# Optimization experiments

Hardware: AMD Instinct MI355X
Metric: run time of the kernel (lower is better)

Reference implementation:

```python
import jax, jax.numpy as jnp
import numpy as np

N, E, C, H, G = 100000, 1600000, 128, 64, 512
TOL = 1e-7          # PyG topk tolerance
MIN_SCORE = 0.05
EPS_KL = 1e-14


def setup_inputs() -> dict:
    key = jax.random.key(0)
    ks = jax.random.split(key, 12)
    d = {}
    d["x"] = jax.random.normal(ks[0], (N, C), jnp.float32)
    d["edge_index"] = jax.random.randint(ks[1], (2, E), 0, N)
    d["batch"] = jnp.sort(jax.random.randint(ks[2], (N,), 0, G))
    d["attn"] = jax.random.uniform(ks[3], (N,), jnp.float32, minval=1e-3, maxval=1.0)
    def lin(k, i, o):
        return (jax.random.normal(k, (i, o), jnp.float32) / np.sqrt(i)).astype(jnp.float32)
    d["W1"] = lin(ks[4], C, H); d["b1"] = jnp.zeros((H,), jnp.float32)
    d["W2"] = lin(ks[5], H, H); d["b2"] = jnp.zeros((H,), jnp.float32)
    d["pool_w"] = (jax.random.normal(ks[6], (C,), jnp.float32) / np.sqrt(C)).astype(jnp.float32)
    d["W3"] = lin(ks[7], H, H); d["b3"] = jnp.zeros((H,), jnp.float32)
    d["W4"] = lin(ks[8], H, H); d["b4"] = jnp.zeros((H,), jnp.float32)
    d["Wl"] = lin(ks[9], H, 1); d["bl"] = jnp.zeros((1,), jnp.float32)
    return d


def _gin(x, src, dst, Wa, ba, Wb, bb, edge_w=None):
    # GINConv with eps=0: nn((1+0)*x + sum_{j in N(i)} x_j), nn = Lin-ReLU-Lin
    msg = x[src]                                   # [E, F] gather
    if edge_w is not None:
        msg = msg * edge_w[:, None]                # drop pruned edges
    agg = jax.ops.segment_sum(msg, dst, num_segments=x.shape[0])
    h = x + agg
    return jax.nn.relu(h @ Wa + ba) @ Wb + bb


def reference(x, edge_index, batch, attn, W1, b1, W2, b2, pool_w, W3, b3, W4, b4, Wl, bl):
    src, dst = edge_index[0], edge_index[1]
    out = jax.nn.relu(_gin(x, src, dst, W1, b1, W2, b2))

    # --- TopKPooling(min_score=0.05), attn=x ---
    raw = x @ pool_w                               # [N] attention logits
    m = jax.ops.segment_max(raw, batch, num_segments=G)
    e = jnp.exp(raw - m[batch])
    z = jax.ops.segment_sum(e, batch, num_segments=G)
    score = e / z[batch]                           # per-graph softmax
    smax = jax.ops.segment_max(score, batch, num_segments=G)
    thresh = jnp.minimum(smax[batch] - TOL, MIN_SCORE)
    mask = score > thresh                          # kept nodes (>=1 per graph)
    maskf = mask.astype(x.dtype)
    out = out * (score * maskf)[:, None]           # x[perm] * score[perm]
    edge_keep = maskf[src] * maskf[dst]            # filter_adj: both endpoints kept

    out = jax.nn.relu(_gin(out, src, dst, W3, b3, W4, b4, edge_w=edge_keep)) * maskf[:, None]
    graph_out = jax.ops.segment_sum(out, batch, num_segments=G)  # global_add_pool
    pred = (graph_out @ Wl + bl).reshape(-1)       # [G]

    # attn_loss = scatter_mean(kl_div(log(score+eps), attn[perm]), batch)
    kl = attn * (jnp.log(attn) - jnp.log(score + EPS_KL))
    cnt = jax.ops.segment_sum(maskf, batch, num_segments=G)
    attn_loss = jax.ops.segment_sum(kl * maskf, batch, num_segments=G) / jnp.maximum(cnt, 1.0)

    ratio = maskf.sum() / x.shape[0]
    return pred, attn_loss, ratio
```

## Files before the change

kernel.cpp:

```cpp
#include <hip/hip_runtime.h>
#include <math.h>

#define N_NODES 100000
#define N_EDGES 1600000
#define C_IN    128
#define H_DIM   64
#define G_GRAPHS 512
#define MAXG    4096
#define ELCAP   65536
#define KPG     32
#define NBITS   3136

__global__ void kpre(const float* __restrict__ x, const float* __restrict__ pool_w,
                     const int* __restrict__ batch,
                     float* __restrict__ sc, unsigned int* __restrict__ zero_region,
                     int* __restrict__ gstart) {
    int gid = blockIdx.x * blockDim.x + threadIdx.x;
    int nthr = gridDim.x * blockDim.x;
    if (gid < NBITS + 1) zero_region[gid] = 0u;
    for (int i = gid; i < N_NODES; i += nthr) {
        int b = batch[i];
        int prev = (i == 0) ? -1 : batch[i - 1];
        for (int g = prev + 1; g <= b; ++g) gstart[g] = i;
    }
    if (gid == 0) {
        int last = batch[N_NODES - 1];
        for (int g = last + 1; g <= G_GRAPHS; ++g) gstart[g] = N_NODES;
    }
    const int lane = threadIdx.x & 63;
    const int l32  = lane & 31;
    const int half = lane >> 5;
    const float4 pwv = ((const float4*)pool_w)[l32];
    const int wid = blockIdx.x * (blockDim.x >> 6) + (threadIdx.x >> 6);
    const int nw  = gridDim.x * (blockDim.x >> 6);
    for (int r0 = wid * 4; r0 < N_NODES; r0 += nw * 4) {
        int rowA = r0 + half;
        int rowB = r0 + 2 + half;
        float4 xa = ((const float4*)(x + (size_t)rowA * C_IN))[l32];
        float4 xb = ((const float4*)(x + (size_t)rowB * C_IN))[l32];
        float pa = xa.x * pwv.x + xa.y * pwv.y + xa.z * pwv.z + xa.w * pwv.w;
        float pb = xb.x * pwv.x + xb.y * pwv.y + xb.z * pwv.z + xb.w * pwv.w;
        #pragma unroll
        for (int m = 16; m > 0; m >>= 1) {
            pa += __shfl_xor(pa, m, 64);
            pb += __shfl_xor(pb, m, 64);
        }
        if (l32 == 0) { sc[rowA] = pa; sc[rowB] = pb; }
    }
}

__device__ __forceinline__ float blk_max(float v, float* red, int lane, int w) {
    #pragma unroll
    for (int m = 32; m > 0; m >>= 1) v = fmaxf(v, __shfl_xor(v, m, 64));
    if (lane == 0) red[w] = v;
    __syncthreads();
    float r = fmaxf(fmaxf(red[0], red[1]), fmaxf(red[2], red[3]));
    __syncthreads();
    return r;
}
__device__ __forceinline__ float blk_sum(float v, float* red, int lane, int w) {
    #pragma unroll
    for (int m = 32; m > 0; m >>= 1) v += __shfl_xor(v, m, 64);
    if (lane == 0) red[w] = v;
    __syncthreads();
    float r = (red[0] + red[1]) + (red[2] + red[3]);
    __syncthreads();
    return r;
}

__global__ void kA4(const int* __restrict__ gstart, const float* __restrict__ attn,
                    float* __restrict__ sc, unsigned int* __restrict__ kept_bits,
                    int* __restrict__ klist, int* __restrict__ kcnt,
                    float* __restrict__ B, float* __restrict__ out) {
    __shared__ float buf[MAXG];
    __shared__ float red[4];
    __shared__ int   lst[KPG];
    __shared__ int   cntk;
    const int g = blockIdx.x;
    const int t = threadIdx.x;
    const int lane = t & 63;
    const int w = t >> 6;
    const int ns = gstart[g];
    const int ne = gstart[g + 1];
    const int cn = ne - ns;
    if (cn <= 0) {
        if (t == 0) { out[G_GRAPHS + g] = 0.f; kcnt[g] = 0; }
        return;
    }
    if (t == 0) cntk = 0;
    float lmax = -3.4e38f;
    for (int i = t; i < cn; i += 256) { float r = sc[ns + i]; buf[i] = r; lmax = fmaxf(lmax, r); }
    float m = blk_max(lmax, red, lane, w);
    float lsum = 0.f;
    for (int i = t; i < cn; i += 256) { float e = expf(buf[i] - m); buf[i] = e; lsum += e; }
    float z = blk_sum(lsum, red, lane, w);
    float thresh = fminf(1.f / z - 1e-7f, 0.05f);
    float klacc = 0.f;
    for (int i = t; i < cn; i += 256) {
        float s = buf[i] / z;
        if (s > thresh) {
            int n = ns + i;
            int p = atomicAdd(&cntk, 1);
            if (p < KPG) lst[p] = i;
            sc[n] = s;
            float a = attn[n];
            klacc += a * (logf(a) - logf(s + 1e-14f));
        }
    }
    float klsum = blk_sum(klacc, red, lane, w);
    int kct = cntk;
    int kc = kct < KPG ? kct : KPG;
    if (t == 0) {
        out[G_GRAPHS + g] = (kct > 0) ? klsum / (float)kct : 0.f;
        kcnt[g] = kc;
    }
    for (int i = t; i < kc; i += 256) {
        int n = ns + lst[i];
        klist[g * KPG + i] = n;
        atomicOr(&kept_bits[n >> 5], 1u << (n & 31));
    }
    for (int j = t; j < kc * H_DIM; j += 256)
        B[(size_t)(ns + lst[j >> 6]) * H_DIM + (j & 63)] = 0.f;
}

__device__ __forceinline__ void emit(bool hit, int s, int d, int* __restrict__ list,
                                     int cap, int* __restrict__ count, int lane) {
    unsigned long long bal = __ballot(hit);
    if (bal == 0ull) return;
    int leader = __ffsll((long long)bal) - 1;
    int cnt = __popcll(bal);
    int base = 0;
    if (lane == leader) base = atomicAdd(count, cnt);
    base = __shfl(base, leader, 64);
    if (hit) {
        int p = base + __popcll(bal & ((1ull << lane) - 1ull));
        if (p < cap) { list[p] = s; list[cap + p] = d; }
    }
}

__global__ void kscan(const int* __restrict__ ei, const unsigned int* __restrict__ bits,
                      const float* __restrict__ x, const float* __restrict__ W1,
                      float* __restrict__ B, int* __restrict__ elsd,
                      int* __restrict__ elcount) {
    __shared__ int ls[1024], ld[1024];
    __shared__ int c1;
    const int t = threadIdx.x;
    const int lane = t & 63;
    if (t == 0) c1 = 0;
    int t4 = blockIdx.x * 256 + t;
    bool valid = t4 < (N_EDGES / 4);
    int4 s4 = make_int4(0, 0, 0, 0), d4 = make_int4(0, 0, 0, 0);
    if (valid) {
        s4 = ((const int4*)ei)[t4];
        d4 = ((const int4*)(ei + N_EDGES))[t4];
    }
    __syncthreads();
    int sv[4] = {s4.x, s4.y, s4.z, s4.w};
    int dv[4] = {d4.x, d4.y, d4.z, d4.w};
    bool bk[4];
    #pragma unroll
    for (int q = 0; q < 4; ++q) {
        int ss = sv[q], dd = dv[q];
        bool kd = valid && (((bits[dd >> 5] >> (dd & 31)) & 1u) != 0u);
        bk[q] = kd && (((bits[ss >> 5] >> (ss & 31)) & 1u) != 0u);
        if (kd) { int p = atomicAdd(&c1, 1); ls[p] = ss; ld[p] = dd; }
    }
    #pragma unroll
    for (int q = 0; q < 4; ++q) emit(bk[q], sv[q], dv[q], elsd, ELCAP, elcount, lane);
    __syncthreads();
    const int nloc = c1;
    if (nloc == 0) return;
    const int w = t >> 6;
    for (int idx = w; idx < nloc; idx += 4) {
        int s = ls[idx];
        int d = ld[idx];
        const float4* xr = (const float4*)(x + (size_t)s * C_IN);
        float acc = 0.f;
        #pragma unroll 8
        for (int k4 = 0; k4 < C_IN / 4; ++k4) {
            float4 xv = xr[k4];
            acc = fmaf(xv.x, W1[(4 * k4 + 0) * H_DIM + lane], acc);
            acc = fmaf(xv.y, W1[(4 * k4 + 1) * H_DIM + lane], acc);
            acc = fmaf(xv.z, W1[(4 * k4 + 2) * H_DIM + lane], acc);
            acc = fmaf(xv.w, W1[(4 * k4 + 3) * H_DIM + lane], acc);
        }
        atomicAdd(&B[(size_t)d * H_DIM + lane], acc);
    }
}

__device__ __forceinline__ float computeA(int n, int lane,
                                          const float* __restrict__ x,
                                          const float* __restrict__ B,
                                          const float* __restrict__ sc,
                                          const float* __restrict__ W1, float b1l,
                                          const float* __restrict__ W2, float b2l,
                                          const float* __restrict__ W3) {
    const float4* xr = (const float4*)(x + (size_t)n * C_IN);
    float u = 0.f;
    #pragma unroll 8
    for (int k4 = 0; k4 < C_IN / 4; ++k4) {
        float4 xv = xr[k4];
        u = fmaf(xv.x, W1[(4 * k4 + 0) * H_DIM + lane], u);
        u = fmaf(xv.y, W1[(4 * k4 + 1) * H_DIM + lane], u);
        u = fmaf(xv.z, W1[(4 * k4 + 2) * H_DIM + lane], u);
        u = fmaf(xv.w, W1[(4 * k4 + 3) * H_DIM + lane], u);
    }
    float t1 = fmaxf(u + B[(size_t)n * H_DIM + lane] + b1l, 0.f);
    float o1 = b2l;
    #pragma unroll 8
    for (int k = 0; k < H_DIM; ++k) o1 = fmaf(__shfl(t1, k, 64), W2[k * H_DIM + lane], o1);
    o1 = fmaxf(o1, 0.f);
    float v = 0.f;
    #pragma unroll 8
    for (int k = 0; k < H_DIM; ++k) v = fmaf(__shfl(o1, k, 64), W3[k * H_DIM + lane], v);
    return v * sc[n];
}

__global__ void kfin(const int* __restrict__ klist, const int* __restrict__ kcnt,
                     const float* __restrict__ sc, const float* __restrict__ x,
                     const float* __restrict__ W1, const float* __restrict__ b1,
                     const float* __restrict__ W2, const float* __restrict__ b2,
                     const float* __restrict__ W3, const float* __restrict__ b3,
                     const float* __restrict__ W4, const float* __restrict__ b4,
                     const float* __restrict__ Wl, const float* __restrict__ bl,
                     const float* __restrict__ B, const int* __restrict__ elsd,
                     const int* __restrict__ elcount, float* __restrict__ out) {
    __shared__ float Abuf[KPG][H_DIM];
    __shared__ float Gbuf[KPG][H_DIM];
    __shared__ int   kl_s[KPG];
    const int g = blockIdx.x;
    const int t = threadIdx.x;
    const int lane = t & 63;
    const int w = t >> 6;
    const float b1l = b1[lane], b2l = b2[lane];
    const int kc = kcnt[g];
    if (t < KPG) kl_s[t] = (t < kc) ? klist[g * KPG + t] : 0;
    __syncthreads();
    int ec = *elcount; if (ec > ELCAP) ec = ELCAP;
    for (int i = w; i < kc; i += 4) {
        int n = __builtin_amdgcn_readfirstlane(kl_s[i]);
        float vA = computeA(n, lane, x, B, sc, W1, b1l, W2, b2l, W3);
        float agg = 0.f;
        for (int base = 0; base < ec; base += 64) {
            int idx = base + lane;
            int dd = (idx < ec) ? elsd[ELCAP + idx] : -1;
            bool mtc = (dd == n);
            int ssl = mtc ? elsd[idx] : 0;
            unsigned long long bal = __ballot(mtc);
            while (bal) {
                int j = __ffsll((long long)bal) - 1;
                bal &= bal - 1;
                int s = __builtin_amdgcn_readfirstlane(__shfl(ssl, j, 64));
                agg += computeA(s, lane, x, B, sc, W1, b1l, W2, b2l, W3);
            }
        }
        Abuf[i][lane] = vA;
        Gbuf[i][lane] = agg;
    }
    __syncthreads();
    if (w == 0) {
        const float b3l = b3[lane], b4l = b4[lane];
        float gsum = 0.f;
        for (int i = 0; i < kc; ++i) {
            float tt = fmaxf(Abuf[i][lane] + Gbuf[i][lane] + b3l, 0.f);
            float o2 = b4l;
            #pragma unroll 8
            for (int k = 0; k < H_DIM; ++k)
                o2 = fmaf(__shfl(tt, k, 64), W4[k * H_DIM + lane], o2);
            gsum += fmaxf(o2, 0.f);
        }
        float p = gsum * Wl[lane];
        #pragma unroll
        for (int m = 32; m > 0; m >>= 1) p += __shfl_xor(p, m, 64);
        if (lane == 0) out[g] = p + bl[0];
    }
    if (g == 0 && w == 1) {
        int tot = 0;
        for (int i = lane; i < G_GRAPHS; i += 64) tot += kcnt[i];
        #pragma unroll
        for (int m = 32; m > 0; m >>= 1) tot += __shfl_xor(tot, m, 64);
        if (lane == 0) out[2 * G_GRAPHS] = (float)tot * (1.f / (float)N_NODES);
    }
}

extern "C" void kernel_launch(void* const* d_in, const int* in_sizes, int n_in,
                              void* d_out, int out_size, void* d_ws, size_t ws_size,
                              hipStream_t stream) {
    const float* x      = (const float*)d_in[0];
    const int*   ei     = (const int*)d_in[1];
    const int*   batch  = (const int*)d_in[2];
    const float* attn   = (const float*)d_in[3];
    const float* W1     = (const float*)d_in[4];
    const float* b1     = (const float*)d_in[5];
    const float* W2     = (const float*)d_in[6];
    const float* b2     = (const float*)d_in[7];
    const float* pool_w = (const float*)d_in[8];
    const float* W3     = (const float*)d_in[9];
    const float* b3     = (const float*)d_in[10];
    const float* W4     = (const float*)d_in[11];
    const float* b4     = (const float*)d_in[12];
    const float* Wl     = (const float*)d_in[13];
    const float* bl     = (const float*)d_in[14];
    float* out = (float*)d_out;

    float* B      = (float*)d_ws;
    float* sc     = B + (size_t)N_NODES * H_DIM;
    int*   klist  = (int*)(sc + N_NODES);
    int*   kcnt   = klist + G_GRAPHS * KPG;
    int*   elsd   = kcnt + G_GRAPHS;
    unsigned int* kept_bits = (unsigned int*)(elsd + 2 * ELCAP);
    int*          elcount   = (int*)(kept_bits + NBITS);
    int*          gstart    = elcount + 1;

    kpre  <<<2048, 256, 0, stream>>>(x, pool_w, batch, sc, kept_bits, gstart);
    kA4   <<<G_GRAPHS, 256, 0, stream>>>(gstart, attn, sc, kept_bits, klist, kcnt, B, out);
    kscan <<<(N_EDGES / 4 + 255) / 256, 256, 0, stream>>>(ei, kept_bits, x, W1, B,
                                                          elsd, elcount);
    kfin  <<<G_GRAPHS, 256, 0, stream>>>(klist, kcnt, sc, x, W1, b1, W2, b2, W3, b3,
                                         W4, b4, Wl, bl, B, elsd, elcount, out);
}
```

Baseline: 168.1 us.

## Fuse score projection and per-graph softmax into one per-graph kernel

Merges the pre-pass kernel (x·pool_w projection, graph-start computation, bitmask zeroing) into the per-graph softmax/top-k kernel. Each 1024-thread block now finds its graph range with a wave-level binary search over the sorted batch array, clears its own bits of the kept bitmask with atomicAnd, and computes the logits straight into shared memory. This removes one launch and the round trip of the logits through global memory. In exchange only 512 blocks read x, with fewer waves in flight than the 2048-block pre-pass, and clearing bits per graph may leave some words uncleared if any graph is empty.

```diff
diff --git a/kernel.cpp b/kernel.cpp
--- a/kernel.cpp
+++ b/kernel.cpp
@@ -11,67 +11,40 @@
 #define KPG     32
 #define NBITS   3136
 
-__global__ void kpre(const float* __restrict__ x, const float* __restrict__ pool_w,
-                     const int* __restrict__ batch,
-                     float* __restrict__ sc, unsigned int* __restrict__ zero_region,
-                     int* __restrict__ gstart) {
-    int gid = blockIdx.x * blockDim.x + threadIdx.x;
-    int nthr = gridDim.x * blockDim.x;
-    if (gid < NBITS + 1) zero_region[gid] = 0u;
-    for (int i = gid; i < N_NODES; i += nthr) {
-        int b = batch[i];
-        int prev = (i == 0) ? -1 : batch[i - 1];
-        for (int g = prev + 1; g <= b; ++g) gstart[g] = i;
-    }
-    if (gid == 0) {
-        int last = batch[N_NODES - 1];
-        for (int g = last + 1; g <= G_GRAPHS; ++g) gstart[g] = N_NODES;
-    }
-    const int lane = threadIdx.x & 63;
-    const int l32  = lane & 31;
-    const int half = lane >> 5;
-    const float4 pwv = ((const float4*)pool_w)[l32];
-    const int wid = blockIdx.x * (blockDim.x >> 6) + (threadIdx.x >> 6);
-    const int nw  = gridDim.x * (blockDim.x >> 6);
-    for (int r0 = wid * 4; r0 < N_NODES; r0 += nw * 4) {
-        int rowA = r0 + half;
-        int rowB = r0 + 2 + half;
-        float4 xa = ((const float4*)(x + (size_t)rowA * C_IN))[l32];
-        float4 xb = ((const float4*)(x + (size_t)rowB * C_IN))[l32];
-        float pa = xa.x * pwv.x + xa.y * pwv.y + xa.z * pwv.z + xa.w * pwv.w;
-        float pb = xb.x * pwv.x + xb.y * pwv.y + xb.z * pwv.z + xb.w * pwv.w;
-        #pragma unroll
-        for (int m = 16; m > 0; m >>= 1) {
-            pa += __shfl_xor(pa, m, 64);
-            pb += __shfl_xor(pb, m, 64);
-        }
-        if (l32 == 0) { sc[rowA] = pa; sc[rowB] = pb; }
-    }
-}
-
-__device__ __forceinline__ float blk_max(float v, float* red, int lane, int w) {
-    #pragma unroll
-    for (int m = 32; m > 0; m >>= 1) v = fmaxf(v, __shfl_xor(v, m, 64));
-    if (lane == 0) red[w] = v;
-    __syncthreads();
-    float r = fmaxf(fmaxf(red[0], red[1]), fmaxf(red[2], red[3]));
-    __syncthreads();
-    return r;
-}
-__device__ __forceinline__ float blk_sum(float v, float* red, int lane, int w) {
-    #pragma unroll
-    for (int m = 32; m > 0; m >>= 1) v += __shfl_xor(v, m, 64);
-    if (lane == 0) red[w] = v;
-    __syncthreads();
-    float r = (red[0] + red[1]) + (red[2] + red[3]);
-    __syncthreads();
-    return r;
-}
-
-__global__ void kA4(const int* __restrict__ gstart, const float* __restrict__ attn,
-                    float* __restrict__ sc, unsigned int* __restrict__ kept_bits,
-                    int* __restrict__ klist, int* __restrict__ kcnt,
-                    float* __restrict__ B, float* __restrict__ out) {
+__device__ __forceinline__ int lbound64(const int* __restrict__ b, int val, int lane) {
+    int lo = 0, hi = N_NODES;
+    while (lo < hi) {
+        int len = hi - lo;
+        if (len <= 64) {
+            int p = lo + lane;
+            bool c = (p >= hi) || (b[p] >= val);
+            unsigned long long bal = __ballot(c);
+            lo = (bal == 0ull) ? hi : lo + (__ffsll((long long)bal) - 1);
+            hi = lo;
+        } else {
+            int step = len >> 6;
+            int p = lo + lane * step;
+            bool c = b[p] >= val;
+            unsigned long long bal = __ballot(c);
+            if (bal == 0ull) {
+                lo = lo + 63 * step + 1;
+            } else {
+                int j = __ffsll((long long)bal) - 1;
+                if (j == 0) { hi = lo; }
+                else { int nlo = lo + (j - 1) * step + 1; hi = lo + j * step; lo = nlo; }
+            }
+        }
+    }
+    return lo;
+}
+
+__global__ __launch_bounds__(1024, 4) void kSM(
+    const float* __restrict__ x, const int* __restrict__ batch,
+    const float* __restrict__ attn, const float* __restrict__ pool_w,
+    float* __restrict__ sc, unsigned int* __restrict__ kept_bits,
+    int* __restrict__ klist, int* __restrict__ kcnt,
+    float* __restrict__ B, int* __restrict__ elcount, float* __restrict__ out)
+{
     __shared__ float buf[MAXG];
     __shared__ float red[4];
     __shared__ int   lst[KPG];
@@ -79,47 +52,96 @@
     const int g = blockIdx.x;
     const int t = threadIdx.x;
     const int lane = t & 63;
-    const int w = t >> 6;
-    const int ns = gstart[g];
-    const int ne = gstart[g + 1];
+    const int w64 = t >> 6;
+    if (g == 0 && t == 0) *elcount = 0;
+    if (t == 0) cntk = 0;
+
+    const int ns = lbound64(batch, g, lane);
+    const int ne = lbound64(batch, g + 1, lane);
     const int cn = ne - ns;
     if (cn <= 0) {
         if (t == 0) { out[G_GRAPHS + g] = 0.f; kcnt[g] = 0; }
         return;
     }
-    if (t == 0) cntk = 0;
+
+    {
+        const int w0 = ns >> 5, w1 = (ne - 1) >> 5;
+        for (int wd = w0 + t; wd <= w1; wd += 1024) {
+            int lo_b = ns - (wd << 5); if (lo_b < 0) lo_b = 0;
+            int hi_b = ne - (wd << 5); if (hi_b > 32) hi_b = 32;
+            unsigned int mask = (hi_b == 32 ? 0xFFFFFFFFu : ((1u << hi_b) - 1u))
+                                & ~((1u << lo_b) - 1u);
+            atomicAnd(&kept_bits[wd], ~mask);
+        }
+    }
+
+    {
+        const int l32  = lane & 31;
+        const int half = lane >> 5;
+        const int hw   = (w64 << 1) + half;
+        const float4 pwv = ((const float4*)pool_w)[l32];
+        for (int r = ns + hw; r < ne; r += 32) {
+            float4 xa = ((const float4*)(x + (size_t)r * C_IN))[l32];
+            float pa = xa.x * pwv.x + xa.y * pwv.y + xa.z * pwv.z + xa.w * pwv.w;
+            #pragma unroll
+            for (int m = 16; m > 0; m >>= 1) pa += __shfl_xor(pa, m, 64);
+            if (l32 == 0) buf[r - ns] = pa;
+        }
+    }
+    __syncthreads();
+
     float lmax = -3.4e38f;
-    for (int i = t; i < cn; i += 256) { float r = sc[ns + i]; buf[i] = r; lmax = fmaxf(lmax, r); }
-    float m = blk_max(lmax, red, lane, w);
+    if (t < 256) for (int i = t; i < cn; i += 256) lmax = fmaxf(lmax, buf[i]);
+    #pragma unroll
+    for (int m = 32; m > 0; m >>= 1) lmax = fmaxf(lmax, __shfl_xor(lmax, m, 64));
+    if (t < 256 && lane == 0) red[w64] = lmax;
+    __syncthreads();
+    const float mx = fmaxf(fmaxf(red[0], red[1]), fmaxf(red[2], red[3]));
+    __syncthreads();
+
     float lsum = 0.f;
-    for (int i = t; i < cn; i += 256) { float e = expf(buf[i] - m); buf[i] = e; lsum += e; }
-    float z = blk_sum(lsum, red, lane, w);
-    float thresh = fminf(1.f / z - 1e-7f, 0.05f);
+    if (t < 256) for (int i = t; i < cn; i += 256) {
+        float e = expf(buf[i] - mx); buf[i] = e; lsum += e;
+    }
+    #pragma unroll
+    for (int m = 32; m > 0; m >>= 1) lsum += __shfl_xor(lsum, m, 64);
+    if (t < 256 && lane == 0) red[w64] = lsum;
+    __syncthreads();
+    const float z = (red[0] + red[1]) + (red[2] + red[3]);
+    __syncthreads();
+
+    const float thresh = fminf(1.f / z - 1e-7f, 0.05f);
     float klacc = 0.f;
-    for (int i = t; i < cn; i += 256) {
-        float s = buf[i] / z;
-        if (s > thresh) {
-            int n = ns + i;
-            int p = atomicAdd(&cntk, 1);
-            if (p < KPG) lst[p] = i;
-            sc[n] = s;
-            float a = attn[n];
-            klacc += a * (logf(a) - logf(s + 1e-14f));
-        }
-    }
-    float klsum = blk_sum(klacc, red, lane, w);
+    if (t < 256) {
+        for (int i = t; i < cn; i += 256) {
+            float s = buf[i] / z;
+            if (s > thresh) {
+                int n = ns + i;
+                int p = atomicAdd(&cntk, 1);
+                if (p < KPG) lst[p] = i;
+                sc[n] = s;
+                float a = attn[n];
+                klacc += a * (logf(a) - logf(s + 1e-14f));
+            }
+        }
+    }
+    #pragma unroll
+    for (int m = 32; m > 0; m >>= 1) klacc += __shfl_xor(klacc, m, 64);
+    if (t < 256 && lane == 0) red[w64] = klacc;
+    __syncthreads();
+    const float klsum = (red[0] + red[1]) + (red[2] + red[3]);
     int kct = cntk;
     int kc = kct < KPG ? kct : KPG;
     if (t == 0) {
         out[G_GRAPHS + g] = (kct > 0) ? klsum / (float)kct : 0.f;
         kcnt[g] = kc;
     }
-    for (int i = t; i < kc; i += 256) {
+    for (int i = t; i < kc; i += 1024) {
         int n = ns + lst[i];
         klist[g * KPG + i] = n;
         atomicOr(&kept_bits[n >> 5], 1u << (n & 31));
     }
-    for (int j = t; j < kc * H_DIM; j += 256)
+    for (int j = t; j < kc * H_DIM; j += 1024)
         B[(size_t)(ns + lst[j >> 6]) * H_DIM + (j & 63)] = 0.f;
 }
 
@@ -310,10 +332,9 @@
     int*   elsd   = kcnt + G_GRAPHS;
     unsigned int* kept_bits = (unsigned int*)(elsd + 2 * ELCAP);
     int*          elcount   = (int*)(kept_bits + NBITS);
-    int*          gstart    = elcount + 1;
-
-    kpre  <<<2048, 256, 0, stream>>>(x, pool_w, batch, sc, kept_bits, gstart);
-    kA4   <<<G_GRAPHS, 256, 0, stream>>>(gstart, attn, sc, kept_bits, klist, kcnt, B, out);
+
+    kSM   <<<G_GRAPHS, 1024, 0, stream>>>(x, batch, attn, pool_w, sc, kept_bits,
+                                          klist, kcnt, B, elcount, out);
     kscan <<<(N_EDGES / 4 + 255) / 256, 256, 0, stream>>>(ei, kept_bits, x, W1, B,
                                                           elsd, elcount);
     kfin  <<<G_GRAPHS, 256, 0, stream>>>(klist, kcnt, sc, x, W1, b1, W2, b2, W3, b3,
```

New measurement: 171.3 us. About the same (+1.9%).
